# Optimization experiments

Hardware: AMD Instinct MI355X
Metric: run time of the kernel (lower is better)

The kernel has to match this reference:

```python
import jax, jax.numpy as jnp
import numpy as np

B, T, HID, H, Dk, Dv, K = 2, 1024, 1024, 8, 128, 128, 4
EPS = 1e-5


def _dwconv_causal(y, w, b):
    # y: [B,T,C], w: [C,1,K], b: [C]; torch Conv1d(padding=K-1) then [:, :, :T] == causal left-pad
    C = y.shape[-1]
    z = jnp.transpose(y, (0, 2, 1))  # [B,C,T]
    z = jax.lax.conv_general_dilated(
        z, w, window_strides=(1,), padding=[(K - 1, 0)],
        feature_group_count=C, dimension_numbers=("NCH", "OIH", "NCH"))
    z = z + b[None, :, None]
    return jnp.transpose(z, (0, 2, 1))


def _forward(x, Wq, Wk, Wv, conv_q_w, conv_q_b, conv_k_w, conv_k_b,
             conv_v_w, conv_v_b, Wa, ba, Wb, bb, Wg, Wo, ln_g, ln_b):
    b_, t_ = x.shape[0], x.shape[1]
    q = jax.nn.silu(_dwconv_causal(x @ Wq, conv_q_w, conv_q_b))
    k = jax.nn.silu(_dwconv_causal(x @ Wk, conv_k_w, conv_k_b))
    v = jax.nn.silu(_dwconv_causal(x @ Wv, conv_v_w, conv_v_b))
    q = q.reshape(b_, t_, H, Dk)
    k = k.reshape(b_, t_, H, Dk) * (Dk ** -0.5)
    v = v.reshape(b_, t_, H, Dv)
    alpha = jax.nn.sigmoid(x @ Wa + ba)  # [B,T,H]
    beta = jax.nn.sigmoid(x @ Wb + bb)   # [B,T,H]

    # time-major for scan
    qt = jnp.transpose(q, (1, 0, 2, 3))  # [T,B,H,Dk]
    kt = jnp.transpose(k, (1, 0, 2, 3))
    vt = jnp.transpose(v, (1, 0, 2, 3))  # [T,B,H,Dv]
    at = jnp.transpose(alpha, (1, 0, 2))  # [T,B,H]
    bt = jnp.transpose(beta, (1, 0, 2))

    def step(S, inp):
        q_t, k_t, v_t, a_t, b_t = inp
        sk = jnp.einsum('bhij,bhj->bhi', S, k_t)          # S @ k
        err = sk - v_t                                     # [B,H,Dv]
        S = a_t[:, :, None, None] * S - b_t[:, :, None, None] * (err[..., None] * k_t[:, :, None, :])
        o_t = jnp.einsum('bhij,bhj->bhi', S, q_t)          # S @ q (post-update)
        return S, o_t

    S0 = jnp.zeros((b_, H, Dv, Dk), x.dtype)
    _, o = jax.lax.scan(step, S0, (qt, kt, vt, at, bt))
    o = jnp.transpose(o, (1, 0, 2, 3))  # [B,T,H,Dv]

    # LayerNorm over Dv
    mu = jnp.mean(o, axis=-1, keepdims=True)
    var = jnp.mean((o - mu) ** 2, axis=-1, keepdims=True)
    o = (o - mu) * jax.lax.rsqrt(var + EPS) * ln_g + ln_b

    g = jax.nn.sigmoid(x @ Wg).reshape(b_, t_, H, Dv)
    o = (o * g).reshape(b_, t_, H * Dv)
    return o @ Wo


def setup_inputs() -> dict:
    key = jax.random.key(0)
    ks = jax.random.split(key, 18)
    s = 0.02

    def n(k, shape, scale=s):
        return jax.random.normal(k, shape, jnp.float32) * scale

    return {
        "x": jax.random.normal(ks[0], (B, T, HID), jnp.float32),
        "Wq": n(ks[1], (HID, H * Dk)),
        "Wk": n(ks[2], (HID, H * Dk)),
        "Wv": n(ks[3], (HID, H * Dv)),
        "conv_q_w": n(ks[4], (H * Dk, 1, K), 0.25),
        "conv_q_b": n(ks[5], (H * Dk,), 0.1),
        "conv_k_w": n(ks[6], (H * Dk, 1, K), 0.25),
        "conv_k_b": n(ks[7], (H * Dk,), 0.1),
        "conv_v_w": n(ks[8], (H * Dv, 1, K), 0.25),
        "conv_v_b": n(ks[9], (H * Dv,), 0.1),
        "Wa": n(ks[10], (HID, H)),
        "ba": n(ks[11], (H,), 0.1),
        "Wb": n(ks[12], (HID, H)),
        "bb": n(ks[13], (H,), 0.1),
        "Wg": n(ks[14], (HID, H * Dv)),
        "Wo": n(ks[15], (H * Dv, HID)),
        "ln_g": jnp.ones((Dv,), jnp.float32),
        "ln_b": jnp.zeros((Dv,), jnp.float32),
    }


def reference(x, Wq, Wk, Wv, conv_q_w, conv_q_b, conv_k_w, conv_k_b,
              conv_v_w, conv_v_b, Wa, ba, Wb, bb, Wg, Wo, ln_g, ln_b):
    return _forward(x, Wq, Wk, Wv, conv_q_w, conv_q_b, conv_k_w, conv_k_b,
                    conv_v_w, conv_v_b, Wa, ba, Wb, bb, Wg, Wo, ln_g, ln_b)
```

## Files before the change

### kernel.cpp

```cpp
#include <hip/hip_runtime.h>

#define TSEQ 1024
#define HID_ 1024
#define NH 8
#define DK 128
#define DV 128
#define ROWS 2048
#define SZf (ROWS * HID_)
#define LCH 64
#define NCK 16
#define KSTR 136
#define ESTR 65

typedef __attribute__((ext_vector_type(8))) short short8;
typedef __attribute__((ext_vector_type(4))) float f32x4;
#define MFMA __builtin_amdgcn_mfma_f32_16x16x32_bf16

__device__ __forceinline__ float sig_(float x) { return 1.f / (1.f + __expf(-x)); }

__device__ __forceinline__ ushort f2bf(float f) {
    unsigned int u = __builtin_bit_cast(unsigned int, f);
    u += 0x7FFF + ((u >> 16) & 1);
    return (ushort)(u >> 16);
}
__device__ __forceinline__ float bf2f(ushort u) {
    return __builtin_bit_cast(float, ((unsigned int)u) << 16);
}
__device__ __forceinline__ unsigned int pk2(float lo, float hi) {
    return (unsigned int)f2bf(lo) | ((unsigned int)f2bf(hi) << 16);
}

__device__ __forceinline__ void gload16(const void* g, void* l) {
    __builtin_amdgcn_global_load_lds(
        (const __attribute__((address_space(1))) unsigned int*)g,
        (__attribute__((address_space(3))) unsigned int*)l, 16, 0, 0);
}

__global__ __launch_bounds__(256)
void k_x2bf(const float* __restrict__ x, ushort* __restrict__ xb)
{
    const size_t i8 = (size_t)blockIdx.x * 256 + threadIdx.x;
    float4 v0 = *(const float4*)(x + i8 * 8);
    float4 v1 = *(const float4*)(x + i8 * 8 + 4);
    uint4 o;
    o.x = pk2(v0.x, v0.y); o.y = pk2(v0.z, v0.w);
    o.z = pk2(v1.x, v1.y); o.w = pk2(v1.z, v1.w);
    *(uint4*)(xb + i8 * 8) = o;
}

__global__ __launch_bounds__(256)
void k_wT(const float* __restrict__ s0, const float* __restrict__ s1,
          const float* __restrict__ s2, const float* __restrict__ s3,
          ushort* __restrict__ dst)
{
    const int z = blockIdx.z;
    const float* W = (z == 0) ? s0 : (z == 1) ? s1 : (z == 2) ? s2 : s3;
    ushort* WT = dst + (size_t)z * (1024 * 1024);
    __shared__ float t[64][65];
    const int n0 = blockIdx.x * 64, k0 = blockIdx.y * 64;
    const int rr = threadIdx.x >> 4, cc = threadIdx.x & 15;
#pragma unroll
    for (int i = 0; i < 4; ++i) {
        const int row = i * 16 + rr;
        float4 v = *(const float4*)(W + (size_t)(k0 + row) * 1024 + n0 + cc * 4);
        t[row][cc * 4 + 0] = v.x; t[row][cc * 4 + 1] = v.y;
        t[row][cc * 4 + 2] = v.z; t[row][cc * 4 + 3] = v.w;
    }
    __syncthreads();
#pragma unroll
    for (int i = 0; i < 4; ++i) {
        const int n = i * 16 + rr;
        const int kc = cc * 4;
        ushort4 o;
        o.x = f2bf(t[kc + 0][n]); o.y = f2bf(t[kc + 1][n]);
        o.z = f2bf(t[kc + 2][n]); o.w = f2bf(t[kc + 3][n]);
        *(ushort4*)(WT + (size_t)(n0 + n) * 1024 + k0 + kc) = o;
    }
}

__device__ __forceinline__ void gemm_tile_mfma(const ushort* __restrict__ A,
                                               const ushort* __restrict__ BT,
                                               float* __restrict__ C,
                                               int brow, int bcol)
{
    __shared__ ushort As[128 * 32];
    __shared__ ushort Bs[128 * 32];
    const int tid  = threadIdx.x;
    const int lane = tid & 63;
    const int wv   = tid >> 6;
    const int wm   = (wv >> 1) * 64;
    const int wn   = (wv & 1) * 64;
    const int l15  = lane & 15;
    const int k8   = (lane >> 4) * 8;
    const int row0 = (tid >> 2);
    const int q0   = (tid & 3) * 8;

    f32x4 acc[4][4];
#pragma unroll
    for (int i = 0; i < 4; ++i)
#pragma unroll
        for (int j = 0; j < 4; ++j)
#pragma unroll
            for (int e = 0; e < 4; ++e) acc[i][j][e] = 0.f;

    for (int k0 = 0; k0 < 1024; k0 += 32) {
        __syncthreads();
#pragma unroll
        for (int j = 0; j < 2; ++j) {
            const int i   = j * 256 + tid;
            const int row = j * 64 + row0;
            const int i0  = j * 256 + wv * 64;
            gload16(A  + (size_t)(brow + row) * 1024 + k0 + q0, As + i0 * 8);
            gload16(BT + (size_t)(bcol + row) * 1024 + k0 + q0, Bs + i0 * 8);
            (void)i;
        }
        __syncthreads();
        short8 af[4], bf[4];
#pragma unroll
        for (int i = 0; i < 4; ++i)
            af[i] = *(const short8*)(As + (wm + i * 16 + l15) * 32 + k8);
#pragma unroll
        for (int j = 0; j < 4; ++j)
            bf[j] = *(const short8*)(Bs + (wn + j * 16 + l15) * 32 + k8);
#pragma unroll
        for (int i = 0; i < 4; ++i)
#pragma unroll
            for (int j = 0; j < 4; ++j)
                acc[i][j] = MFMA(af[i], bf[j], acc[i][j], 0, 0, 0);
    }
    const int l4 = lane >> 4;
#pragma unroll
    for (int i = 0; i < 4; ++i)
#pragma unroll
        for (int j = 0; j < 4; ++j)
#pragma unroll
            for (int r = 0; r < 4; ++r)
                C[(size_t)(brow + wm + i * 16 + l4 * 4 + r) * 1024 +
                  bcol + wn + j * 16 + l15] = acc[i][j][r];
}

__global__ __launch_bounds__(256)
void k_gemm4(const ushort* __restrict__ A, const ushort* __restrict__ WT,
             float* __restrict__ Cbase)
{
    const ushort* BT = WT + (size_t)blockIdx.z * (1024 * 1024);
    float* C = Cbase + (size_t)blockIdx.z * SZf;
    gemm_tile_mfma(A, BT, C, blockIdx.y * 128, blockIdx.x * 128);
}

__global__ __launch_bounds__(256)
void k_gemm1(const ushort* __restrict__ A, const ushort* __restrict__ BT,
             float* __restrict__ C)
{
    gemm_tile_mfma(A, BT, C, blockIdx.y * 128, blockIdx.x * 128);
}

__global__ __launch_bounds__(256)
void k_ab(const float* __restrict__ x, const float* __restrict__ Wa,
          const float* __restrict__ ba, const float* __restrict__ Wb,
          const float* __restrict__ bb, float* __restrict__ aT,
          float* __restrict__ bT)
{
    const int r = blockIdx.x * 4 + (threadIdx.x >> 6);
    const int lane = threadIdx.x & 63;
    const int b = r >> 10, t = r & 1023;
    const float* xr = x + (size_t)r * HID_;
    float acc[16];
#pragma unroll
    for (int n = 0; n < 16; ++n) acc[n] = 0.f;
    for (int c = lane; c < HID_; c += 64) {
        const float xv = xr[c];
        const float* wa = Wa + c * 8;
        const float* wb = Wb + c * 8;
#pragma unroll
        for (int n = 0; n < 8; ++n) {
            acc[n]     = fmaf(xv, wa[n], acc[n]);
            acc[8 + n] = fmaf(xv, wb[n], acc[8 + n]);
        }
    }
#pragma unroll
    for (int n = 0; n < 16; ++n) {
#pragma unroll
        for (int m = 32; m; m >>= 1) acc[n] += __shfl_xor(acc[n], m);
    }
    if (lane < 8) {
        aT[(size_t)(b * 8 + lane) * TSEQ + t] = sig_(acc[lane] + ba[lane]);
        bT[(size_t)(b * 8 + lane) * TSEQ + t] = sig_(acc[8 + lane] + bb[lane]);
    }
}

__global__ __launch_bounds__(256)
void k_conv_save(const float* __restrict__ q, const float* __restrict__ k,
                 const float* __restrict__ v, float* __restrict__ scr)
{
    const int z = blockIdx.z, b = blockIdx.y, j = blockIdx.x + 1;
    const float* y = (z == 0) ? q : (z == 1) ? k : v;
    float* d = scr + ((size_t)(z * 2 + b) * 15 + (j - 1)) * 3 * 1024;
    const float* s = y + ((size_t)b * TSEQ + j * 64 - 3) * HID_;
    for (int i = threadIdx.x; i < 3 * 1024; i += 256)
        d[i] = s[i];
}

__global__ __launch_bounds__(256)
void k_conv_apply(float* __restrict__ q, float* __restrict__ k, float* __restrict__ v,
                  const float* __restrict__ scr,
                  const float* __restrict__ wq, const float* __restrict__ bq,
                  const float* __restrict__ wk, const float* __restrict__ bk,
                  const float* __restrict__ wv, const float* __restrict__ bv)
{
    const int z = blockIdx.z, b = blockIdx.y;
    const int j = blockIdx.x >> 2, cg = blockIdx.x & 3;
    float* y          = (z == 0) ? q  : (z == 1) ? k  : v;
    const float* w    = (z == 0) ? wq : (z == 1) ? wk : wv;
    const float* bias = (z == 0) ? bq : (z == 1) ? bk : bv;
    const float scale = (z == 1) ? 0.08838834764831845f : 1.f;
    const int c = cg * 256 + threadIdx.x;
    const float w0 = w[c * 4], w1 = w[c * 4 + 1], w2 = w[c * 4 + 2], w3 = w[c * 4 + 3];
    const float bs = bias[c];
    float y0 = 0.f, y1 = 0.f, y2 = 0.f;
    if (j > 0) {
        const float* s = scr + ((size_t)(z * 2 + b) * 15 + (j - 1)) * 3 * 1024 + c;
        y0 = s[0]; y1 = s[1024]; y2 = s[2048];
    }
    float* yp = y + ((size_t)b * TSEQ + j * 64) * HID_ + c;
#pragma unroll 4
    for (int t = 0; t < 64; ++t) {
        float y3  = yp[(size_t)t * HID_];
        float acc = fmaf(w0, y0, fmaf(w1, y1, fmaf(w2, y2, fmaf(w3, y3, bs))));
        float sv  = acc * sig_(acc) * scale;
        yp[(size_t)t * HID_] = sv;
        y0 = y1; y1 = y2; y2 = y3;
    }
}

__global__ __launch_bounds__(256)
void k_stageprep(const float* __restrict__ klin, const float* __restrict__ qlin,
                 const float* __restrict__ vlin,
                 const float* __restrict__ aT, const float* __restrict__ bT,
                 ushort* __restrict__ Kst, ushort* __restrict__ Qst,
                 ushort* __restrict__ Vst, ushort* __restrict__ KTst,
                 ushort* __restrict__ Mg, ushort* __restrict__ Gg,
                 float* __restrict__ pug, float* __restrict__ pog,
                 float* __restrict__ cg, float* __restrict__ dtotg)
{
    const int cid = blockIdx.x;
    const int bh = cid >> 4, c = cid & 15;
    const int b = bh >> 3, h = bh & 7;
    const int tid = threadIdx.x;
    const int t0 = c * LCH;

    __shared__ ushort Kb[64 * KSTR], Qb[64 * KSTR];
    __shared__ ushort Vl[128 * 72];
    __shared__ float Ef[64 * ESTR];
    __shared__ float Mf[64 * ESTR];
    __shared__ float cums[64], bv[64];

    if (tid < 64) {
        const float a = aT[(size_t)bh * TSEQ + t0 + tid];
        bv[tid] = bT[(size_t)bh * TSEQ + t0 + tid];
        float cs = __logf(a);
#pragma unroll
        for (int d = 1; d < 64; d <<= 1) {
            float pv = __shfl_up(cs, d);
            if (tid >= d) cs += pv;
        }
        cums[tid] = cs;
    }
    const float* kb = klin + ((size_t)b * TSEQ + t0) * HID_ + h * DK;
    const float* qb = qlin + ((size_t)b * TSEQ + t0) * HID_ + h * DK;
    const float* vb = vlin + ((size_t)b * TSEQ + t0) * HID_ + h * DV;
    const size_t go = (size_t)cid * 8192;
#pragma unroll
    for (int j = 0; j < 8; ++j) {
        const int i4 = tid + j * 256;
        const int row = i4 >> 5, c4 = i4 & 31;
        float4 kv = *(const float4*)(kb + (size_t)row * HID_ + c4 * 4);
        float4 qv = *(const float4*)(qb + (size_t)row * HID_ + c4 * 4);
        float4 vv = *(const float4*)(vb + (size_t)row * HID_ + c4 * 4);
        uint2 kp; kp.x = pk2(kv.x, kv.y); kp.y = pk2(kv.z, kv.w);
        uint2 qp; qp.x = pk2(qv.x, qv.y); qp.y = pk2(qv.z, qv.w);
        *(uint2*)(Kst + go + row * 128 + c4 * 4) = kp;
        *(uint2*)(Qst + go + row * 128 + c4 * 4) = qp;
        *(uint2*)(Kb + row * KSTR + c4 * 4) = kp;
        *(uint2*)(Qb + row * KSTR + c4 * 4) = qp;
        const int dv0 = c4 * 4;
        Vl[(dv0 + 0) * 72 + row] = f2bf(vv.x);
        Vl[(dv0 + 1) * 72 + row] = f2bf(vv.y);
        Vl[(dv0 + 2) * 72 + row] = f2bf(vv.z);
        Vl[(dv0 + 3) * 72 + row] = f2bf(vv.w);
    }
    __syncthreads();

#pragma unroll
    for (int j = 0; j < 4; ++j) {
        const int idx = tid + j * 256;
        const int dv = idx >> 3, tq = (idx & 7) * 8;
        *(uint4*)(Vst + go + dv * 64 + tq) = *(const uint4*)(Vl + dv * 72 + tq);
        const int dk = idx >> 3, tt = (idx & 7) * 8;
        ushort tmp[8];
#pragma unroll
        for (int e = 0; e < 8; ++e) tmp[e] = Kb[(tt + e) * KSTR + dk];
        *(uint4*)(KTst + go + dk * 64 + tt) = *(uint4*)tmp;
    }

    const int wv = tid >> 6, l = tid & 63, l15 = l & 15, lq = l >> 4;
    const int k8o = lq * 8;
    f32x4 accK[4], accQ4[4];
#pragma unroll
    for (int j = 0; j < 4; ++j) {
        accK[j] = f32x4{0.f, 0.f, 0.f, 0.f};
        accQ4[j] = f32x4{0.f, 0.f, 0.f, 0.f};
    }
#pragma unroll
    for (int kk = 0; kk < 4; ++kk) {
        short8 aK = *(const short8*)(Kb + (wv * 16 + l15) * KSTR + kk * 32 + k8o);
        short8 aQ = *(const short8*)(Qb + (wv * 16 + l15) * KSTR + kk * 32 + k8o);
#pragma unroll
        for (int js = 0; js < 4; ++js) {
            short8 bK = *(const short8*)(Kb + (js * 16 + l15) * KSTR + kk * 32 + k8o);
            accK[js]  = MFMA(aK, bK, accK[js], 0, 0, 0);
            accQ4[js] = MFMA(aQ, bK, accQ4[js], 0, 0, 0);
        }
    }
    ushort* Gc = Gg + (size_t)cid * 4096;
#pragma unroll
    for (int js = 0; js < 4; ++js) {
#pragma unroll
        for (int r = 0; r < 4; ++r) {
            const int t = wv * 16 + lq * 4 + r;
            const int s = js * 16 + l15;
            const float cp = (t > 0) ? cums[t - 1] : 0.f;
            Ef[t * ESTR + s] = (s < t) ? __expf(cp - cums[s]) * accK[js][r] : 0.f;
            const float gv = (s <= t) ? __expf(cums[t] - cums[s]) * accQ4[js][r] : 0.f;
            Gc[t * 64 + s] = f2bf(gv);
        }
    }
    __syncthreads();

    if (tid < 64) {
        const int s = tid;
        for (int r = 0; r < 64; ++r) Mf[r * ESTR + s] = 0.f;
        Mf[s * ESTR + s] = bv[s];
        for (int t = 1; t < 64; ++t) {
            float s0 = 0.f, s1 = 0.f;
            int r = 0;
            for (; r + 1 < t; r += 2) {
                s0 = fmaf(Ef[t * ESTR + r],     Mf[r * ESTR + s],       s0);
                s1 = fmaf(Ef[t * ESTR + r + 1], Mf[(r + 1) * ESTR + s], s1);
            }
            if (r < t) s0 = fmaf(Ef[t * ESTR + r], Mf[r * ESTR + s], s0);
            if (s < t) Mf[t * ESTR + s] = -bv[t] * (s0 + s1);
        }
    }
    __syncthreads();
    ushort* Mc = Mg + (size_t)cid * 4096;
#pragma unroll
    for (int j = 0; j < 16; ++j) {
        const int e = tid + j * 256;
        Mc[e] = f2bf(Mf[(e >> 6) * ESTR + (e & 63)]);
    }
    if (tid < 64) {
        const float cp = (tid > 0) ? cums[tid - 1] : 0.f;
        pug[cid * 64 + tid] = __expf(cp);
        pog[cid * 64 + tid] = __expf(cums[tid]);
        cg [cid * 64 + tid] = __expf(cums[63] - cums[tid]);
        if (tid == 0) dtotg[cid] = __expf(cums[63]);
    }
}

__global__ __launch_bounds__(256)
void k_scan2(const ushort* __restrict__ Kst, const ushort* __restrict__ KTst,
             const ushort* __restrict__ Vst, const ushort* __restrict__ Mg,
             const float* __restrict__ pug, const float* __restrict__ cgd,
             const float* __restrict__ dtg,
             ushort* __restrict__ Sst, ushort* __restrict__ Wst)
{
    const int blk = blockIdx.x;
    const int bh = blk >> 1, half = blk & 1;
    const int tid = threadIdx.x;
    const int wv = tid >> 6, l = tid & 63, l15 = l & 15, lq = l >> 4;
    const int k8o = lq * 8;
    const int dvw = wv * 16;

    __shared__ ushort Kb[64 * KSTR];
    __shared__ ushort KTb[128 * 72];
    __shared__ ushort Mb[64 * 72];
    __shared__ ushort Vb[64 * 72];
    __shared__ ushort Shb[64 * KSTR], Slb[64 * KSTR];
    __shared__ ushort Yb[64 * 72], Wb[64 * 72], Wcb[64 * 72];
    __shared__ float puv[64], cv2[64], dts[1];

    f32x4 accS[8];
#pragma unroll
    for (int m = 0; m < 8; ++m) accS[m] = f32x4{0.f, 0.f, 0.f, 0.f};

    uint4 rk[4], rkt[4], rm[2], rv[2];
    float rpu = 0.f, rcv = 0.f, rdt = 0.f;

    auto LOADC = [&](int cc) {
        const int cid = bh * 16 + cc;
        const size_t go = (size_t)cid * 8192;
#pragma unroll
        for (int j = 0; j < 4; ++j) {
            rk[j]  = *(const uint4*)(Kst  + go + (tid + j * 256) * 8);
            rkt[j] = *(const uint4*)(KTst + go + (tid + j * 256) * 8);
        }
#pragma unroll
        for (int j = 0; j < 2; ++j) {
            rm[j] = *(const uint4*)(Mg + (size_t)cid * 4096 + (tid + j * 256) * 8);
            rv[j] = *(const uint4*)(Vst + go + half * 4096 + (tid + j * 256) * 8);
        }
        if (tid < 64) {
            rpu = pug[cid * 64 + tid];
            rcv = cgd[cid * 64 + tid];
            if (tid == 0) rdt = dtg[cid];
        }
    };
    auto WRITEC = [&]() {
#pragma unroll
        for (int j = 0; j < 4; ++j) {
            const int i16 = tid + j * 256;
            *(uint4*)(Kb  + (i16 >> 4) * KSTR + (i16 & 15) * 8) = rk[j];
            *(uint4*)(KTb + (i16 >> 3) * 72   + (i16 & 7) * 8)  = rkt[j];
        }
#pragma unroll
        for (int j = 0; j < 2; ++j) {
            const int i8 = tid + j * 256;
            *(uint4*)(Mb + (i8 >> 3) * 72 + (i8 & 7) * 8) = rm[j];
            *(uint4*)(Vb + (i8 >> 3) * 72 + (i8 & 7) * 8) = rv[j];
        }
        if (tid < 64) {
            puv[tid] = rpu; cv2[tid] = rcv;
            if (tid == 0) dts[0] = rdt;
        }
    };

    LOADC(0); WRITEC();
    __syncthreads();

    for (int c = 0; c < NCK; ++c) {
        if (c + 1 < NCK) LOADC(c + 1);

#pragma unroll
        for (int m = 0; m < 8; ++m) {
            ushort h4[4], l4v[4];
#pragma unroll
            for (int r = 0; r < 4; ++r) {
                const float sv = accS[m][r];
                const ushort hi = f2bf(sv);
                h4[r] = hi;
                l4v[r] = f2bf(sv - bf2f(hi));
            }
            *(uint2*)(Shb + (dvw + l15) * KSTR + m * 16 + lq * 4) = *(uint2*)h4;
            *(uint2*)(Slb + (dvw + l15) * KSTR + m * 16 + lq * 4) = *(uint2*)l4v;
        }
        f32x4 accU[4];
#pragma unroll
        for (int jj = 0; jj < 4; ++jj) accU[jj] = f32x4{0.f, 0.f, 0.f, 0.f};
#pragma unroll
        for (int kk = 0; kk < 4; ++kk) {
            short8 sh = *(const short8*)(Shb + (dvw + l15) * KSTR + kk * 32 + k8o);
            short8 sl = *(const short8*)(Slb + (dvw + l15) * KSTR + kk * 32 + k8o);
#pragma unroll
            for (int jj = 0; jj < 4; ++jj) {
                short8 ka = *(const short8*)(Kb + (jj * 16 + l15) * KSTR + kk * 32 + k8o);
                accU[jj] = MFMA(ka, sh, accU[jj], 0, 0, 0);
                accU[jj] = MFMA(ka, sl, accU[jj], 0, 0, 0);
            }
        }
#pragma unroll
        for (int jj = 0; jj < 4; ++jj) {
            float pu4[4];
            *(float4*)pu4 = *(const float4*)(puv + jj * 16 + lq * 4);
            ushort v4[4];
            *(uint2*)v4 = *(const uint2*)(Vb + (dvw + l15) * 72 + jj * 16 + lq * 4);
            ushort y4[4];
#pragma unroll
            for (int r = 0; r < 4; ++r)
                y4[r] = f2bf(bf2f(v4[r]) - pu4[r] * accU[jj][r]);
            *(uint2*)(Yb + (dvw + l15) * 72 + jj * 16 + lq * 4) = *(uint2*)y4;
        }
        f32x4 accW[4];
#pragma unroll
        for (int jj = 0; jj < 4; ++jj) accW[jj] = f32x4{0.f, 0.f, 0.f, 0.f};
#pragma unroll
        for (int kk = 0; kk < 2; ++kk) {
            short8 yb = *(const short8*)(Yb + (dvw + l15) * 72 + kk * 32 + k8o);
#pragma unroll
            for (int jj = 0; jj < 4; ++jj) {
                short8 mf = *(const short8*)(Mb + (jj * 16 + l15) * 72 + kk * 32 + k8o);
                accW[jj] = MFMA(mf, yb, accW[jj], 0, 0, 0);
            }
        }
#pragma unroll
        for (int jj = 0; jj < 4; ++jj) {
            float cv4[4];
            *(float4*)cv4 = *(const float4*)(cv2 + jj * 16 + lq * 4);
            ushort w4[4], wc4[4];
#pragma unroll
            for (int r = 0; r < 4; ++r) {
                const float wl = accW[jj][r];
                w4[r]  = f2bf(wl);
                wc4[r] = f2bf(wl * cv4[r]);
            }
            *(uint2*)(Wb  + (dvw + l15) * 72 + jj * 16 + lq * 4) = *(uint2*)w4;
            *(uint2*)(Wcb + (dvw + l15) * 72 + jj * 16 + lq * 4) = *(uint2*)wc4;
        }
        const float dt = dts[0];
#pragma unroll
        for (int m = 0; m < 8; ++m)
#pragma unroll
            for (int r = 0; r < 4; ++r) accS[m][r] *= dt;
#pragma unroll
        for (int kk = 0; kk < 2; ++kk) {
            short8 wc = *(const short8*)(Wcb + (dvw + l15) * 72 + kk * 32 + k8o);
#pragma unroll
            for (int m = 0; m < 8; ++m) {
                short8 kt = *(const short8*)(KTb + (m * 16 + l15) * 72 + kk * 32 + k8o);
                accS[m] = MFMA(kt, wc, accS[m], 0, 0, 0);
            }
        }
        {
            const int cid = bh * 16 + c;
#pragma unroll
            for (int j = 0; j < 4; ++j) {
                const int idx = l + j * 64;
                const int dvo = idx >> 4, ko = (idx & 15) * 8;
                *(uint4*)(Sst + (size_t)cid * 16384 +
                          (half * 64 + dvw + dvo) * 128 + ko) =
                    *(const uint4*)(Shb + (dvw + dvo) * KSTR + ko);
            }
#pragma unroll
            for (int j = 0; j < 2; ++j) {
                const int idx = l + j * 64;
                const int dvo = idx >> 3, t8 = (idx & 7) * 8;
                *(uint4*)(Wst + (size_t)cid * 8192 +
                          (half * 64 + dvw + dvo) * 64 + t8) =
                    *(const uint4*)(Wb + (dvw + dvo) * 72 + t8);
            }
        }
        __syncthreads();
        if (c + 1 < NCK) WRITEC();
        __syncthreads();
    }
}

__global__ __launch_bounds__(256)
void k_out(const ushort* __restrict__ Sst, const ushort* __restrict__ Qst,
           const ushort* __restrict__ Gg, const ushort* __restrict__ Wst,
           const float* __restrict__ pog, const float* __restrict__ g_lin,
           const float* __restrict__ lng, const float* __restrict__ lnb,
           ushort* __restrict__ ogb)
{
    const int cid = blockIdx.x;
    const int bh = cid >> 4, c = cid & 15;
    const int b = bh >> 3, h = bh & 7;
    const int t0 = c * LCH;
    const int tid = threadIdx.x;
    const int wv = tid >> 6, l = tid & 63, l15 = l & 15, lq = l >> 4;
    const int k8o = lq * 8;

    __shared__ ushort Sb[128 * KSTR];
    __shared__ ushort Qb[64 * KSTR];
    __shared__ ushort Gb[64 * 72];
    __shared__ ushort Wqb[128 * 72];
    __shared__ float  Ot[64 * 132];
    __shared__ float  pov[64];

#pragma unroll
    for (int j = 0; j < 8; ++j) {
        const int i16 = tid + j * 256;
        *(uint4*)(Sb + (i16 >> 4) * KSTR + (i16 & 15) * 8) =
            *(const uint4*)(Sst + (size_t)cid * 16384 + i16 * 8);
    }
#pragma unroll
    for (int j = 0; j < 4; ++j) {
        const int i16 = tid + j * 256;
        *(uint4*)(Qb + (i16 >> 4) * KSTR + (i16 & 15) * 8) =
            *(const uint4*)(Qst + (size_t)cid * 8192 + i16 * 8);
        const int i8 = i16;
        *(uint4*)(Wqb + (i8 >> 3) * 72 + (i8 & 7) * 8) =
            *(const uint4*)(Wst + (size_t)cid * 8192 + i8 * 8);
    }
#pragma unroll
    for (int j = 0; j < 2; ++j) {
        const int i8 = tid + j * 256;
        *(uint4*)(Gb + (i8 >> 3) * 72 + (i8 & 7) * 8) =
            *(const uint4*)(Gg + (size_t)cid * 4096 + i8 * 8);
    }
    if (tid < 64) pov[tid] = pog[cid * 64 + tid];
    __syncthreads();

#pragma unroll
    for (int i = 0; i < 2; ++i) {
        const int dvt = wv * 2 + i;
        f32x4 acc[4], acg[4];
#pragma unroll
        for (int jj = 0; jj < 4; ++jj) {
            acc[jj] = f32x4{0.f, 0.f, 0.f, 0.f};
            acg[jj] = f32x4{0.f, 0.f, 0.f, 0.f};
        }
#pragma unroll
        for (int kk = 0; kk < 4; ++kk) {
            short8 sa = *(const short8*)(Sb + (dvt * 16 + l15) * KSTR + kk * 32 + k8o);
#pragma unroll
            for (int jj = 0; jj < 4; ++jj) {
                short8 qb = *(const short8*)(Qb + (jj * 16 + l15) * KSTR + kk * 32 + k8o);
                acc[jj] = MFMA(sa, qb, acc[jj], 0, 0, 0);
            }
        }
#pragma unroll
        for (int kk = 0; kk < 2; ++kk) {
            short8 wa = *(const short8*)(Wqb + (dvt * 16 + l15) * 72 + kk * 32 + k8o);
#pragma unroll
            for (int jj = 0; jj < 4; ++jj) {
                short8 gb = *(const short8*)(Gb + (jj * 16 + l15) * 72 + kk * 32 + k8o);
                acg[jj] = MFMA(wa, gb, acg[jj], 0, 0, 0);
            }
        }
#pragma unroll
        for (int jj = 0; jj < 4; ++jj) {
            const int t = jj * 16 + l15;
            const float po = pov[t];
            float4 o4;
            o4.x = po * acc[jj][0] + acg[jj][0];
            o4.y = po * acc[jj][1] + acg[jj][1];
            o4.z = po * acc[jj][2] + acg[jj][2];
            o4.w = po * acc[jj][3] + acg[jj][3];
            *(float4*)(Ot + t * 132 + dvt * 16 + lq * 4) = o4;
        }
    }
    __syncthreads();

    const int d = l * 2;
    const float lg0 = lng[d], lg1 = lng[d + 1];
    const float lb0 = lnb[d], lb1 = lnb[d + 1];
    const size_t btbase = (size_t)b * TSEQ + t0 + wv * 16;
#pragma unroll 1
    for (int rr = 0; rr < 16; ++rr) {
        const int t = wv * 16 + rr;
        float2 xv = *(const float2*)(Ot + t * 132 + d);
        float s = xv.x + xv.y;
#pragma unroll
        for (int m = 32; m; m >>= 1) s += __shfl_xor(s, m);
        const float mu = s * (1.f / 128.f);
        const float d0 = xv.x - mu, d1 = xv.y - mu;
        float v = d0 * d0 + d1 * d1;
#pragma unroll
        for (int m = 32; m; m >>= 1) v += __shfl_xor(v, m);
        const float inv = rsqrtf(v * (1.f / 128.f) + 1e-5f);
        const float* gp = g_lin + (btbase + rr) * HID_ + h * DV;
        const float g0 = sig_(gp[d]), g1 = sig_(gp[d + 1]);
        const float y0 = (d0 * inv * lg0 + lb0) * g0;
        const float y1 = (d1 * inv * lg1 + lb1) * g1;
        *(uint*)(ogb + (btbase + rr) * HID_ + h * DV + d) = pk2(y0, y1);
    }
}

extern "C" void kernel_launch(void* const* d_in, const int* in_sizes, int n_in,
                              void* d_out, int out_size, void* d_ws, size_t ws_size,
                              hipStream_t stream)
{
    const float* x   = (const float*)d_in[0];
    const float* Wq  = (const float*)d_in[1];
    const float* Wk  = (const float*)d_in[2];
    const float* Wv  = (const float*)d_in[3];
    const float* cqw = (const float*)d_in[4];
    const float* cqb = (const float*)d_in[5];
    const float* ckw = (const float*)d_in[6];
    const float* ckb = (const float*)d_in[7];
    const float* cvw = (const float*)d_in[8];
    const float* cvb = (const float*)d_in[9];
    const float* Wa  = (const float*)d_in[10];
    const float* ba  = (const float*)d_in[11];
    const float* Wb  = (const float*)d_in[12];
    const float* bb  = (const float*)d_in[13];
    const float* Wg  = (const float*)d_in[14];
    const float* Wo  = (const float*)d_in[15];
    const float* lng = (const float*)d_in[16];
    const float* lnb = (const float*)d_in[17];
    float* out = (float*)d_out;
    float* ws  = (float*)d_ws;

    float* q_lin = ws;
    float* k_lin = ws + 1 * (size_t)SZf;
    float* v_lin = ws + 2 * (size_t)SZf;
    float* g_lin = ws + 3 * (size_t)SZf;
    float* o_buf = ws + 4 * (size_t)SZf;
    float* aT    = ws + 5 * (size_t)SZf;
    float* bT    = aT + 16 * TSEQ;
    float* pug   = bT + 16 * TSEQ;
    float* pog   = pug + 256 * 64;
    float* cgd   = pog + 256 * 64;
    float* dtg   = cgd + 256 * 64;

    float*  tail = ws + 5 * (size_t)SZf + 131072;
    ushort* Kst  = (ushort*)tail;
    ushort* Qst  = Kst + (size_t)256 * 8192;
    ushort* xbf  = Qst + (size_t)256 * 8192;
    ushort* Vst  = xbf;
    ushort* KTst = xbf + (size_t)256 * 8192;

    ushort* WT4 = (ushort*)o_buf;
    ushort* WoT = (ushort*)k_lin;
    ushort* ogb = (ushort*)q_lin;
    ushort* Sst = (ushort*)o_buf;
    ushort* Mg  = (ushort*)out;
    ushort* Gg  = Mg + (size_t)256 * 4096;
    ushort* Wst = Gg + (size_t)256 * 4096;

    k_x2bf<<<1024, 256, 0, stream>>>(x, xbf);
    k_wT<<<dim3(16, 16, 4), 256, 0, stream>>>(Wq, Wk, Wv, Wg, WT4);
    k_gemm4<<<dim3(8, 16, 4), 256, 0, stream>>>(xbf, WT4, ws);
    k_ab<<<512, 256, 0, stream>>>(x, Wa, ba, Wb, bb, aT, bT);
    k_conv_save<<<dim3(15, 2, 3), 256, 0, stream>>>(q_lin, k_lin, v_lin, o_buf);
    k_conv_apply<<<dim3(64, 2, 3), 256, 0, stream>>>(q_lin, k_lin, v_lin, o_buf,
                                                     cqw, cqb, ckw, ckb, cvw, cvb);
    k_stageprep<<<256, 256, 0, stream>>>(k_lin, q_lin, v_lin, aT, bT,
                                         Kst, Qst, Vst, KTst, Mg, Gg,
                                         pug, pog, cgd, dtg);
    k_wT<<<dim3(16, 16, 1), 256, 0, stream>>>(Wo, Wo, Wo, Wo, WoT);
    k_scan2<<<32, 256, 0, stream>>>(Kst, KTst, Vst, Mg, pug, cgd, dtg, Sst, Wst);
    k_out<<<256, 256, 0, stream>>>(Sst, Qst, Gg, Wst, pog, g_lin, lng, lnb, ogb);
    k_gemm1<<<dim3(8, 16), 256, 0, stream>>>(ogb, WoT, out);
}
```

Before: 231.3 us.

## Fuse conv with bf16 staging, fold decay into KT, widen GEMM K-tile with swizzle

The causal conv now runs as a single kernel that reads the fp32 projections and writes bf16 chunk-staged Q/K plus row-major bf16 V directly. This replaces the separate save, apply and fp32-to-bf16 staging passes and removes one fp32 round trip through global memory. The per-chunk decay factor is folded into the transposed K inside stageprep, so the scan no longer builds a second scaled W tile or loads the cg array. The shared GEMM tile moves to a K-step of 64 with an XOR-swizzled LDS layout, halving barrier-separated iterations and reducing bank conflicts. Pre-scaling K before bf16 rounding changes where rounding happens and may shift numerics slightly.

```diff
diff --git a/kernel.cpp b/kernel.cpp
--- a/kernel.cpp
+++ b/kernel.cpp
@@ -83,17 +83,15 @@
                                                float* __restrict__ C,
                                                int brow, int bcol)
 {
-    __shared__ ushort As[128 * 32];
-    __shared__ ushort Bs[128 * 32];
+    __shared__ ushort As[128 * 64];
+    __shared__ ushort Bs[128 * 64];
     const int tid  = threadIdx.x;
     const int lane = tid & 63;
     const int wv   = tid >> 6;
     const int wm   = (wv >> 1) * 64;
     const int wn   = (wv & 1) * 64;
     const int l15  = lane & 15;
-    const int k8   = (lane >> 4) * 8;
-    const int row0 = (tid >> 2);
-    const int q0   = (tid & 3) * 8;
+    const int lq   = lane >> 4;
 
     f32x4 acc[4][4];
 #pragma unroll
@@ -103,30 +101,37 @@
 #pragma unroll
             for (int e = 0; e < 4; ++e) acc[i][j][e] = 0.f;
 
-    for (int k0 = 0; k0 < 1024; k0 += 32) {
+    for (int k0 = 0; k0 < 1024; k0 += 64) {
         __syncthreads();
 #pragma unroll
-        for (int j = 0; j < 2; ++j) {
-            const int i   = j * 256 + tid;
-            const int row = j * 64 + row0;
-            const int i0  = j * 256 + wv * 64;
-            gload16(A  + (size_t)(brow + row) * 1024 + k0 + q0, As + i0 * 8);
-            gload16(BT + (size_t)(bcol + row) * 1024 + k0 + q0, Bs + i0 * 8);
-            (void)i;
+        for (int j = 0; j < 4; ++j) {
+            const int idx  = j * 256 + tid;
+            const int row  = idx >> 3;
+            const int gcol = ((idx & 7) ^ (row & 7)) * 8;
+            const int ldst = (j * 256 + wv * 64) * 8;
+            gload16(A  + (size_t)(brow + row) * 1024 + k0 + gcol, As + ldst);
+            gload16(BT + (size_t)(bcol + row) * 1024 + k0 + gcol, Bs + ldst);
         }
         __syncthreads();
-        short8 af[4], bf[4];
-#pragma unroll
-        for (int i = 0; i < 4; ++i)
-            af[i] = *(const short8*)(As + (wm + i * 16 + l15) * 32 + k8);
-#pragma unroll
-        for (int j = 0; j < 4; ++j)
-            bf[j] = *(const short8*)(Bs + (wn + j * 16 + l15) * 32 + k8);
-#pragma unroll
-        for (int i = 0; i < 4; ++i)
-#pragma unroll
-            for (int j = 0; j < 4; ++j)
-                acc[i][j] = MFMA(af[i], bf[j], acc[i][j], 0, 0, 0);
+#pragma unroll
+        for (int kk = 0; kk < 2; ++kk) {
+            short8 af[4], bf[4];
+#pragma unroll
+            for (int i = 0; i < 4; ++i) {
+                const int ra = wm + i * 16 + l15;
+                af[i] = *(const short8*)(As + ra * 64 + (((kk * 4 + lq) ^ (ra & 7)) * 8));
+            }
+#pragma unroll
+            for (int j = 0; j < 4; ++j) {
+                const int rb = wn + j * 16 + l15;
+                bf[j] = *(const short8*)(Bs + rb * 64 + (((kk * 4 + lq) ^ (rb & 7)) * 8));
+            }
+#pragma unroll
+            for (int i = 0; i < 4; ++i)
+#pragma unroll
+                for (int j = 0; j < 4; ++j)
+                    acc[i][j] = MFMA(af[i], bf[j], acc[i][j], 0, 0, 0);
+        }
     }
     const int l4 = lane >> 4;
 #pragma unroll
@@ -190,58 +195,60 @@
 }
 
 __global__ __launch_bounds__(256)
-void k_conv_save(const float* __restrict__ q, const float* __restrict__ k,
-                 const float* __restrict__ v, float* __restrict__ scr)
-{
-    const int z = blockIdx.z, b = blockIdx.y, j = blockIdx.x + 1;
-    const float* y = (z == 0) ? q : (z == 1) ? k : v;
-    float* d = scr + ((size_t)(z * 2 + b) * 15 + (j - 1)) * 3 * 1024;
-    const float* s = y + ((size_t)b * TSEQ + j * 64 - 3) * HID_;
-    for (int i = threadIdx.x; i < 3 * 1024; i += 256)
-        d[i] = s[i];
-}
-
-__global__ __launch_bounds__(256)
-void k_conv_apply(float* __restrict__ q, float* __restrict__ k, float* __restrict__ v,
-                  const float* __restrict__ scr,
-                  const float* __restrict__ wq, const float* __restrict__ bq,
-                  const float* __restrict__ wk, const float* __restrict__ bk,
-                  const float* __restrict__ wv, const float* __restrict__ bv)
-{
-    const int z = blockIdx.z, b = blockIdx.y;
-    const int j = blockIdx.x >> 2, cg = blockIdx.x & 3;
-    float* y          = (z == 0) ? q  : (z == 1) ? k  : v;
+void k_conv(const float* __restrict__ qf, const float* __restrict__ kf,
+            const float* __restrict__ vf,
+            const float* __restrict__ wq, const float* __restrict__ bq,
+            const float* __restrict__ wk, const float* __restrict__ bk,
+            const float* __restrict__ wv, const float* __restrict__ bv,
+            ushort* __restrict__ Qst, ushort* __restrict__ Kst,
+            ushort* __restrict__ Vrm)
+{
+    const int j = blockIdx.x >> 1, cg = blockIdx.x & 1;
+    const int b = blockIdx.y, z = blockIdx.z;
+    const float* src  = (z == 0) ? qf : (z == 1) ? kf : vf;
     const float* w    = (z == 0) ? wq : (z == 1) ? wk : wv;
     const float* bias = (z == 0) ? bq : (z == 1) ? bk : bv;
     const float scale = (z == 1) ? 0.08838834764831845f : 1.f;
-    const int c = cg * 256 + threadIdx.x;
-    const float w0 = w[c * 4], w1 = w[c * 4 + 1], w2 = w[c * 4 + 2], w3 = w[c * 4 + 3];
-    const float bs = bias[c];
-    float y0 = 0.f, y1 = 0.f, y2 = 0.f;
+    const int c2 = cg * 512 + threadIdx.x * 2;
+    const float w0a = w[c2 * 4],     w1a = w[c2 * 4 + 1], w2a = w[c2 * 4 + 2], w3a = w[c2 * 4 + 3];
+    const float w0b = w[c2 * 4 + 4], w1b = w[c2 * 4 + 5], w2b = w[c2 * 4 + 6], w3b = w[c2 * 4 + 7];
+    const float bsa = bias[c2], bsb = bias[c2 + 1];
+    float ya0 = 0.f, ya1 = 0.f, ya2 = 0.f, yb0 = 0.f, yb1 = 0.f, yb2 = 0.f;
     if (j > 0) {
-        const float* s = scr + ((size_t)(z * 2 + b) * 15 + (j - 1)) * 3 * 1024 + c;
-        y0 = s[0]; y1 = s[1024]; y2 = s[2048];
-    }
-    float* yp = y + ((size_t)b * TSEQ + j * 64) * HID_ + c;
+#pragma unroll
+        for (int i = 0; i < 3; ++i) {
+            float2 t = *(const float2*)(src + (size_t)(b * TSEQ + j * 64 - 3 + i) * HID_ + c2);
+            if (i == 0) { ya0 = t.x; yb0 = t.y; }
+            else if (i == 1) { ya1 = t.x; yb1 = t.y; }
+            else { ya2 = t.x; yb2 = t.y; }
+        }
+    }
+    const int h = c2 >> 7, dk = c2 & 127;
+    const int cid = (b * 8 + h) * 16 + j;
+    ushort* dst = (z == 0) ? Qst : Kst;
 #pragma unroll 4
-    for (int t = 0; t < 64; ++t) {
-        float y3  = yp[(size_t)t * HID_];
-        float acc = fmaf(w0, y0, fmaf(w1, y1, fmaf(w2, y2, fmaf(w3, y3, bs))));
-        float sv  = acc * sig_(acc) * scale;
-        yp[(size_t)t * HID_] = sv;
-        y0 = y1; y1 = y2; y2 = y3;
-    }
-}
-
-__global__ __launch_bounds__(256)
-void k_stageprep(const float* __restrict__ klin, const float* __restrict__ qlin,
-                 const float* __restrict__ vlin,
+    for (int tl = 0; tl < 64; ++tl) {
+        float2 xv = *(const float2*)(src + (size_t)(b * TSEQ + j * 64 + tl) * HID_ + c2);
+        float a0 = fmaf(w0a, ya0, fmaf(w1a, ya1, fmaf(w2a, ya2, fmaf(w3a, xv.x, bsa))));
+        float a1 = fmaf(w0b, yb0, fmaf(w1b, yb1, fmaf(w2b, yb2, fmaf(w3b, xv.y, bsb))));
+        const float s0 = a0 * sig_(a0) * scale;
+        const float s1 = a1 * sig_(a1) * scale;
+        const uint p = pk2(s0, s1);
+        if (z < 2) *(uint*)(dst + (size_t)cid * 8192 + tl * 128 + dk) = p;
+        else       *(uint*)(Vrm + (size_t)(b * TSEQ + j * 64 + tl) * HID_ + c2) = p;
+        ya0 = ya1; ya1 = ya2; ya2 = xv.x;
+        yb0 = yb1; yb1 = yb2; yb2 = xv.y;
+    }
+}
+
+__global__ __launch_bounds__(256)
+void k_stageprep(const ushort* __restrict__ Kst, const ushort* __restrict__ Qst,
+                 const ushort* __restrict__ Vrm,
                  const float* __restrict__ aT, const float* __restrict__ bT,
-                 ushort* __restrict__ Kst, ushort* __restrict__ Qst,
-                 ushort* __restrict__ Vst, ushort* __restrict__ KTst,
+                 ushort* __restrict__ KTst, ushort* __restrict__ VstT,
                  ushort* __restrict__ Mg, ushort* __restrict__ Gg,
                  float* __restrict__ pug, float* __restrict__ pog,
-                 float* __restrict__ cg, float* __restrict__ dtotg)
+                 float* __restrict__ dtotg)
 {
     const int cid = blockIdx.x;
     const int bh = cid >> 4, c = cid & 15;
@@ -266,40 +273,37 @@
         }
         cums[tid] = cs;
     }
-    const float* kb = klin + ((size_t)b * TSEQ + t0) * HID_ + h * DK;
-    const float* qb = qlin + ((size_t)b * TSEQ + t0) * HID_ + h * DK;
-    const float* vb = vlin + ((size_t)b * TSEQ + t0) * HID_ + h * DV;
     const size_t go = (size_t)cid * 8192;
 #pragma unroll
-    for (int j = 0; j < 8; ++j) {
-        const int i4 = tid + j * 256;
-        const int row = i4 >> 5, c4 = i4 & 31;
-        float4 kv = *(const float4*)(kb + (size_t)row * HID_ + c4 * 4);
-        float4 qv = *(const float4*)(qb + (size_t)row * HID_ + c4 * 4);
-        float4 vv = *(const float4*)(vb + (size_t)row * HID_ + c4 * 4);
-        uint2 kp; kp.x = pk2(kv.x, kv.y); kp.y = pk2(kv.z, kv.w);
-        uint2 qp; qp.x = pk2(qv.x, qv.y); qp.y = pk2(qv.z, qv.w);
-        *(uint2*)(Kst + go + row * 128 + c4 * 4) = kp;
-        *(uint2*)(Qst + go + row * 128 + c4 * 4) = qp;
-        *(uint2*)(Kb + row * KSTR + c4 * 4) = kp;
-        *(uint2*)(Qb + row * KSTR + c4 * 4) = qp;
-        const int dv0 = c4 * 4;
-        Vl[(dv0 + 0) * 72 + row] = f2bf(vv.x);
-        Vl[(dv0 + 1) * 72 + row] = f2bf(vv.y);
-        Vl[(dv0 + 2) * 72 + row] = f2bf(vv.z);
-        Vl[(dv0 + 3) * 72 + row] = f2bf(vv.w);
+    for (int j = 0; j < 4; ++j) {
+        const int i16 = tid + j * 256;
+        const int row = i16 >> 4, col = (i16 & 15) * 8;
+        *(uint4*)(Kb + row * KSTR + col) = *(const uint4*)(Kst + go + i16 * 8);
+        *(uint4*)(Qb + row * KSTR + col) = *(const uint4*)(Qst + go + i16 * 8);
+    }
+#pragma unroll
+    for (int j = 0; j < 4; ++j) {
+        const int i16 = tid + j * 256;
+        const int row = i16 >> 4, c8 = (i16 & 15) * 8;
+        ushort tmp[8];
+        *(uint4*)tmp = *(const uint4*)(Vrm + (size_t)(b * TSEQ + t0 + row) * HID_ + h * DV + c8);
+#pragma unroll
+        for (int e = 0; e < 8; ++e)
+            Vl[(c8 + e) * 72 + row] = tmp[e];
     }
     __syncthreads();
 
+    const float ctop = cums[63];
 #pragma unroll
     for (int j = 0; j < 4; ++j) {
         const int idx = tid + j * 256;
         const int dv = idx >> 3, tq = (idx & 7) * 8;
-        *(uint4*)(Vst + go + dv * 64 + tq) = *(const uint4*)(Vl + dv * 72 + tq);
+        *(uint4*)(VstT + go + dv * 64 + tq) = *(const uint4*)(Vl + dv * 72 + tq);
         const int dk = idx >> 3, tt = (idx & 7) * 8;
         ushort tmp[8];
 #pragma unroll
-        for (int e = 0; e < 8; ++e) tmp[e] = Kb[(tt + e) * KSTR + dk];
+        for (int e = 0; e < 8; ++e)
+            tmp[e] = f2bf(bf2f(Kb[(tt + e) * KSTR + dk]) * __expf(ctop - cums[tt + e]));
         *(uint4*)(KTst + go + dk * 64 + tt) = *(uint4*)tmp;
     }
 
@@ -363,16 +367,14 @@
         const float cp = (tid > 0) ? cums[tid - 1] : 0.f;
         pug[cid * 64 + tid] = __expf(cp);
         pog[cid * 64 + tid] = __expf(cums[tid]);
-        cg [cid * 64 + tid] = __expf(cums[63] - cums[tid]);
         if (tid == 0) dtotg[cid] = __expf(cums[63]);
     }
 }
 
 __global__ __launch_bounds__(256)
 void k_scan2(const ushort* __restrict__ Kst, const ushort* __restrict__ KTst,
-             const ushort* __restrict__ Vst, const ushort* __restrict__ Mg,
-             const float* __restrict__ pug, const float* __restrict__ cgd,
-             const float* __restrict__ dtg,
+             const ushort* __restrict__ VstT, const ushort* __restrict__ Mg,
+             const float* __restrict__ pug, const float* __restrict__ dtg,
              ushort* __restrict__ Sst, ushort* __restrict__ Wst)
 {
     const int blk = blockIdx.x;
@@ -387,15 +389,15 @@
     __shared__ ushort Mb[64 * 72];
     __shared__ ushort Vb[64 * 72];
     __shared__ ushort Shb[64 * KSTR], Slb[64 * KSTR];
-    __shared__ ushort Yb[64 * 72], Wb[64 * 72], Wcb[64 * 72];
-    __shared__ float puv[64], cv2[64], dts[1];
+    __shared__ ushort Yb[64 * 72], Wb[64 * 72];
+    __shared__ float puv[64], dts[1];
 
     f32x4 accS[8];
 #pragma unroll
     for (int m = 0; m < 8; ++m) accS[m] = f32x4{0.f, 0.f, 0.f, 0.f};
 
     uint4 rk[4], rkt[4], rm[2], rv[2];
-    float rpu = 0.f, rcv = 0.f, rdt = 0.f;
+    float rpu = 0.f, rdt = 0.f;
 
     auto LOADC = [&](int cc) {
         const int cid = bh * 16 + cc;
@@ -408,11 +410,10 @@
 #pragma unroll
         for (int j = 0; j < 2; ++j) {
             rm[j] = *(const uint4*)(Mg + (size_t)cid * 4096 + (tid + j * 256) * 8);
-            rv[j] = *(const uint4*)(Vst + go + half * 4096 + (tid + j * 256) * 8);
+            rv[j] = *(const uint4*)(VstT + go + half * 4096 + (tid + j * 256) * 8);
         }
         if (tid < 64) {
             rpu = pug[cid * 64 + tid];
-            rcv = cgd[cid * 64 + tid];
             if (tid == 0) rdt = dtg[cid];
         }
     };
@@ -430,7 +431,7 @@
             *(uint4*)(Vb + (i8 >> 3) * 72 + (i8 & 7) * 8) = rv[j];
         }
         if (tid < 64) {
-            puv[tid] = rpu; cv2[tid] = rcv;
+            puv[tid] = rpu;
             if (tid == 0) dts[0] = rdt;
         }
     };
@@ -494,17 +495,11 @@
         }
 #pragma unroll
         for (int jj = 0; jj < 4; ++jj) {
-            float cv4[4];
-            *(float4*)cv4 = *(const float4*)(cv2 + jj * 16 + lq * 4);
-            ushort w4[4], wc4[4];
-#pragma unroll
-            for (int r = 0; r < 4; ++r) {
-                const float wl = accW[jj][r];
-                w4[r]  = f2bf(wl);
-                wc4[r] = f2bf(wl * cv4[r]);
-            }
-            *(uint2*)(Wb  + (dvw + l15) * 72 + jj * 16 + lq * 4) = *(uint2*)w4;
-            *(uint2*)(Wcb + (dvw + l15) * 72 + jj * 16 + lq * 4) = *(uint2*)wc4;
+            ushort w4[4];
+#pragma unroll
+            for (int r = 0; r < 4; ++r)
+                w4[r] = f2bf(accW[jj][r]);
+            *(uint2*)(Wb + (dvw + l15) * 72 + jj * 16 + lq * 4) = *(uint2*)w4;
         }
         const float dt = dts[0];
 #pragma unroll
@@ -513,7 +508,7 @@
             for (int r = 0; r < 4; ++r) accS[m][r] *= dt;
 #pragma unroll
         for (int kk = 0; kk < 2; ++kk) {
-            short8 wc = *(const short8*)(Wcb + (dvw + l15) * 72 + kk * 32 + k8o);
+            short8 wc = *(const short8*)(Wb + (dvw + l15) * 72 + kk * 32 + k8o);
 #pragma unroll
             for (int m = 0; m < 8; ++m) {
                 short8 kt = *(const short8*)(KTb + (m * 16 + l15) * 72 + kk * 32 + k8o);
@@ -691,36 +686,35 @@
     float* bT    = aT + 16 * TSEQ;
     float* pug   = bT + 16 * TSEQ;
     float* pog   = pug + 256 * 64;
-    float* cgd   = pog + 256 * 64;
-    float* dtg   = cgd + 256 * 64;
+    float* dtg   = pog + 256 * 64;
 
     float*  tail = ws + 5 * (size_t)SZf + 131072;
     ushort* Kst  = (ushort*)tail;
     ushort* Qst  = Kst + (size_t)256 * 8192;
     ushort* xbf  = Qst + (size_t)256 * 8192;
-    ushort* Vst  = xbf;
+    ushort* Vrm  = xbf;
     ushort* KTst = xbf + (size_t)256 * 8192;
 
-    ushort* WT4 = (ushort*)o_buf;
-    ushort* WoT = (ushort*)k_lin;
-    ushort* ogb = (ushort*)q_lin;
-    ushort* Sst = (ushort*)o_buf;
-    ushort* Mg  = (ushort*)out;
-    ushort* Gg  = Mg + (size_t)256 * 4096;
-    ushort* Wst = Gg + (size_t)256 * 4096;
+    ushort* WT4  = (ushort*)o_buf;
+    ushort* WoT  = (ushort*)k_lin;
+    ushort* ogb  = (ushort*)q_lin;
+    ushort* VstT = (ushort*)q_lin + (size_t)2 * 1024 * 1024;
+    ushort* Sst  = (ushort*)o_buf;
+    ushort* Mg   = (ushort*)out;
+    ushort* Gg   = Mg + (size_t)256 * 4096;
+    ushort* Wst  = Gg + (size_t)256 * 4096;
 
     k_x2bf<<<1024, 256, 0, stream>>>(x, xbf);
     k_wT<<<dim3(16, 16, 4), 256, 0, stream>>>(Wq, Wk, Wv, Wg, WT4);
     k_gemm4<<<dim3(8, 16, 4), 256, 0, stream>>>(xbf, WT4, ws);
     k_ab<<<512, 256, 0, stream>>>(x, Wa, ba, Wb, bb, aT, bT);
-    k_conv_save<<<dim3(15, 2, 3), 256, 0, stream>>>(q_lin, k_lin, v_lin, o_buf);
-    k_conv_apply<<<dim3(64, 2, 3), 256, 0, stream>>>(q_lin, k_lin, v_lin, o_buf,
-                                                     cqw, cqb, ckw, ckb, cvw, cvb);
-    k_stageprep<<<256, 256, 0, stream>>>(k_lin, q_lin, v_lin, aT, bT,
-                                         Kst, Qst, Vst, KTst, Mg, Gg,
-                                         pug, pog, cgd, dtg);
+    k_conv<<<dim3(32, 2, 3), 256, 0, stream>>>(q_lin, k_lin, v_lin,
+                                               cqw, cqb, ckw, ckb, cvw, cvb,
+                                               Qst, Kst, Vrm);
     k_wT<<<dim3(16, 16, 1), 256, 0, stream>>>(Wo, Wo, Wo, Wo, WoT);
-    k_scan2<<<32, 256, 0, stream>>>(Kst, KTst, Vst, Mg, pug, cgd, dtg, Sst, Wst);
+    k_stageprep<<<256, 256, 0, stream>>>(Kst, Qst, Vrm, aT, bT,
+                                         KTst, VstT, Mg, Gg, pug, pog, dtg);
+    k_scan2<<<32, 256, 0, stream>>>(Kst, KTst, VstT, Mg, pug, dtg, Sst, Wst);
     k_out<<<256, 256, 0, stream>>>(Sst, Qst, Gg, Wst, pog, g_lin, lng, lnb, ogb);
     k_gemm1<<<dim3(8, 16), 256, 0, stream>>>(ogb, WoT, out);
 }
```

New measurement: 217.7 us. -5.9%, faster.
